# Optimization experiments

Hardware: AMD Instinct MI355X
Metric: run time of the kernel (lower is better)

## Reference

```python
import jax, jax.numpy as jnp
import numpy as np

NUM_FREQ = 32
MAX_POS = 10000.0
COORD_DIM = 3
EMB_DIM = COORD_DIM * NUM_FREQ * 2  # 192
KIN = 2 * EMB_DIM                   # 384
C = 32
T = 4
N_Y = 50000
N_X = 32768
K = 8
E = N_X * K
MLP_DIMS = [KIN, 128, 256, 128, C]


def sinusoidal_embed(p):
    # transformer-style sinusoidal embedding: [n, d] -> [n, d*NUM_FREQ*2]
    freqs = (1.0 / MAX_POS) ** (jnp.arange(NUM_FREQ, dtype=p.dtype) / NUM_FREQ)
    ang = p[..., None] * freqs                       # [n, d, nf]
    emb = jnp.stack([jnp.sin(ang), jnp.cos(ang)], axis=-1)  # [n, d, nf, 2]
    return emb.reshape(p.shape[0], -1)


def setup_inputs() -> dict:
    key = jax.random.key(0)
    ks = jax.random.split(key, 16)
    inp = {
        "y": jax.random.uniform(ks[0], (N_Y, COORD_DIM), dtype=jnp.float32),
        "x": jax.random.uniform(ks[1], (N_X, COORD_DIM), dtype=jnp.float32),
        "f_y": jax.random.normal(ks[2], (T, N_Y, C), dtype=jnp.float32),
        "neighbors_index": jax.random.randint(ks[3], (E,), 0, N_Y, dtype=jnp.int64),
    }
    # channel MLP params: 384 -> 128 -> 256 -> 128 -> 32, gelu between layers
    for i in range(4):
        fan_in, fan_out = MLP_DIMS[i], MLP_DIMS[i + 1]
        s = 1.0 / np.sqrt(fan_in)
        inp[f"W{i}"] = jax.random.uniform(ks[4 + 2 * i], (fan_in, fan_out), jnp.float32, -s, s)
        inp[f"b{i}"] = jax.random.uniform(ks[5 + 2 * i], (fan_out,), jnp.float32, -s, s)
    return inp


def reference(y, x, f_y, neighbors_index, W0, b0, W1, b1, W2, b2, W3, b3):
    n_x = x.shape[0]
    k = neighbors_index.shape[0] // n_x
    y_emb = sinusoidal_embed(y)            # [n_y, 192]
    x_emb = sinusoidal_embed(x)            # [n_x, 192]
    rep = y_emb[neighbors_index]           # [E, 192] gather per edge
    slf = jnp.repeat(x_emb, k, axis=0)     # [E, 192] query embedding per edge
    h = jnp.concatenate([rep, slf], axis=-1)  # [E, 384]
    h = jax.nn.gelu(h @ W0 + b0)
    h = jax.nn.gelu(h @ W1 + b1)
    h = jax.nn.gelu(h @ W2 + b2)
    kern = h @ W3 + b3                     # [E, C] kernel values
    in_feat = f_y[:, neighbors_index, :]   # [T, E, C] gathered source features
    prod = kern[None, :, :] * in_feat      # linear transform: k(x,y) * f(y)
    # reduction='sum' over each query's neighborhood (uniform K segments)
    out = prod.reshape(f_y.shape[0], n_x, k, -1).sum(axis=2)  # [T, n_x, C]
    return out
```

## Files before the change

### kernel.cpp

```cpp
#include <hip/hip_runtime.h>
#include <stdint.h>

#define EMB_DIM 192
#define KIN 384
#define CDIM 32
#define TDIM 4
#define N_Y 50000
#define N_X 32768
#define KNBR 8
#define ECNT (N_X*KNBR)

#define AS  200
#define H1S 134
#define H2S 262
#define KS  33

typedef __attribute__((ext_vector_type(8))) short bf16x8;
typedef __attribute__((ext_vector_type(4))) float f32x4;

static __device__ __forceinline__ short f2bf(float f){
  unsigned u = __float_as_uint(f);
  return (short)((u + 0x7FFFu) >> 16);
}
static __device__ __forceinline__ float geluf(float x){
  float x2 = x * x;
  float u  = __builtin_fmaf(0.044715f, x2, 1.0f);
  float p  = x * -1.5957691216057308f;
  float e  = __expf(p * u);
  return x * __builtin_amdgcn_rcpf(1.0f + e);
}

__global__ __launch_bounds__(256) void embed_all(const float* __restrict__ ypts,
                                                 const float* __restrict__ xpts,
                                                 short* __restrict__ emb){
  int id = blockIdx.x * 256 + threadIdx.x;
  int total = (N_Y + N_X) * 96;
  if (id >= total) return;
  int row = id / 96;
  int q = id - row * 96;
  int d = q >> 5, i = q & 31;
  float p = (row < N_Y) ? ypts[row * 3 + d] : xpts[(row - N_Y) * 3 + d];
  float f = __expf(-9.210340371976184f * (float)i * (1.0f / 32.0f));
  float s, c;
  __sincosf(p * f, &s, &c);
  unsigned u0 = __float_as_uint(s), u1 = __float_as_uint(c);
  unsigned pack = ((u0 + 0x7FFFu) >> 16) | (((u1 + 0x7FFFu) >> 16) << 16);
  *(unsigned*)&emb[(size_t)row * EMB_DIM + d * 64 + 2 * i] = pack;
}

__global__ __launch_bounds__(256) void transpose_all(
    const float* __restrict__ W0, const float* __restrict__ W1,
    const float* __restrict__ W2, const float* __restrict__ W3,
    short* __restrict__ w0t, short* __restrict__ w1t,
    short* __restrict__ w2t, short* __restrict__ w3t){
  int id = blockIdx.x * 256 + threadIdx.x;
  const float* src; short* dst; int K, N, loc;
  if      (id < 49152)  { src = W0; dst = w0t; K = 384; N = 128; loc = id; }
  else if (id < 81920)  { src = W1; dst = w1t; K = 128; N = 256; loc = id - 49152; }
  else if (id < 114688) { src = W2; dst = w2t; K = 256; N = 128; loc = id - 81920; }
  else if (id < 118784) { src = W3; dst = w3t; K = 128; N = 32;  loc = id - 114688; }
  else return;
  int n = loc / K, k = loc - n * K;
  dst[n * K + k] = f2bf(src[k * N + n]);
}

__global__ __launch_bounds__(256, 3) void fused_mlp(
    const short* __restrict__ yemb, const short* __restrict__ xemb,
    const int* __restrict__ nidx, const float* __restrict__ f_y,
    const short* __restrict__ w0t, const float* __restrict__ b0,
    const short* __restrict__ w1t, const float* __restrict__ b1,
    const short* __restrict__ w2t, const float* __restrict__ b2,
    const short* __restrict__ w3t, const float* __restrict__ b3,
    float* __restrict__ out)
{
  __shared__ __attribute__((aligned(16))) char smem[50688];
  short* s_a    = (short*)smem;
  short* s_h2   = (short*)smem;
  float* s_kern = (float*)smem;
  short* s_h1   = (short*)(smem + 33536);

  const int tid  = threadIdx.x;
  const int e0   = blockIdx.x * 64;
  const int wave = tid >> 6, lane = tid & 63;
  const int quad = lane >> 4, l15 = lane & 15;

  {
    const int r = tid >> 2, q = tid & 3;
    const int idx_r = nidx[e0 + r];
    const short* yrow = yemb + (size_t)idx_r * EMB_DIM + q * 48;
    uint4 v[6];
    #pragma unroll
    for (int i = 0; i < 6; ++i) v[i] = *(const uint4*)(yrow + i * 8);
    #pragma unroll
    for (int i = 0; i < 6; ++i)
      *(uint4*)&s_a[r * AS + q * 48 + i * 8] = v[i];
  }
  __syncthreads();

  {
    const short* xrow[4];
    #pragma unroll
    for (int mt = 0; mt < 4; ++mt)
      xrow[mt] = xemb + (size_t)((e0 + mt * 16 + l15) >> 3) * EMB_DIM + quad * 8;

    f32x4 acc0[4][2];
    #pragma unroll
    for (int mt = 0; mt < 4; ++mt)
      #pragma unroll
      for (int nt = 0; nt < 2; ++nt) acc0[mt][nt] = (f32x4){0.f, 0.f, 0.f, 0.f};

    #pragma unroll
    for (int ch = 0; ch < 12; ++ch) {
      bf16x8 a[4], b[2];
      #pragma unroll
      for (int mt = 0; mt < 4; ++mt) {
        if (ch < 6) a[mt] = *(const bf16x8*)&s_a[(mt * 16 + l15) * AS + ch * 32 + quad * 8];
        else        a[mt] = *(const bf16x8*)(xrow[mt] + (ch - 6) * 32);
      }
      #pragma unroll
      for (int nt = 0; nt < 2; ++nt)
        b[nt] = *(const bf16x8*)&w0t[(size_t)(wave * 32 + nt * 16 + l15) * 384 + ch * 32 + quad * 8];
      #pragma unroll
      for (int mt = 0; mt < 4; ++mt)
        #pragma unroll
        for (int nt = 0; nt < 2; ++nt)
          acc0[mt][nt] = __builtin_amdgcn_mfma_f32_16x16x32_bf16(a[mt], b[nt], acc0[mt][nt], 0, 0, 0);
    }
    #pragma unroll
    for (int nt = 0; nt < 2; ++nt) {
      int col = wave * 32 + nt * 16 + l15;
      float bias = b0[col];
      #pragma unroll
      for (int mt = 0; mt < 4; ++mt)
        #pragma unroll
        for (int rg = 0; rg < 4; ++rg) {
          int row = mt * 16 + quad * 4 + rg;
          s_h1[row * H1S + col] = f2bf(geluf(acc0[mt][nt][rg] + bias));
        }
    }
  }
  __syncthreads();

  {
    f32x4 acc1[4][4];
    #pragma unroll
    for (int mt = 0; mt < 4; ++mt)
      #pragma unroll
      for (int nt = 0; nt < 4; ++nt) acc1[mt][nt] = (f32x4){0.f, 0.f, 0.f, 0.f};
    #pragma unroll
    for (int ch = 0; ch < 4; ++ch) {
      bf16x8 a[4], b[4];
      #pragma unroll
      for (int mt = 0; mt < 4; ++mt)
        a[mt] = *(const bf16x8*)&s_h1[(mt * 16 + l15) * H1S + ch * 32 + quad * 8];
      #pragma unroll
      for (int nt = 0; nt < 4; ++nt)
        b[nt] = *(const bf16x8*)&w1t[(size_t)(wave * 64 + nt * 16 + l15) * 128 + ch * 32 + quad * 8];
      #pragma unroll
      for (int mt = 0; mt < 4; ++mt)
        #pragma unroll
        for (int nt = 0; nt < 4; ++nt)
          acc1[mt][nt] = __builtin_amdgcn_mfma_f32_16x16x32_bf16(a[mt], b[nt], acc1[mt][nt], 0, 0, 0);
    }
    #pragma unroll
    for (int nt = 0; nt < 4; ++nt) {
      int col = wave * 64 + nt * 16 + l15;
      float bias = b1[col];
      #pragma unroll
      for (int mt = 0; mt < 4; ++mt)
        #pragma unroll
        for (int rg = 0; rg < 4; ++rg) {
          int row = mt * 16 + quad * 4 + rg;
          s_h2[row * H2S + col] = f2bf(geluf(acc1[mt][nt][rg] + bias));
        }
    }
  }
  __syncthreads();

  {
    f32x4 acc2[4][2];
    #pragma unroll
    for (int mt = 0; mt < 4; ++mt)
      #pragma unroll
      for (int nt = 0; nt < 2; ++nt) acc2[mt][nt] = (f32x4){0.f, 0.f, 0.f, 0.f};
    #pragma unroll
    for (int ch = 0; ch < 8; ++ch) {
      bf16x8 a[4], b[2];
      #pragma unroll
      for (int mt = 0; mt < 4; ++mt)
        a[mt] = *(const bf16x8*)&s_h2[(mt * 16 + l15) * H2S + ch * 32 + quad * 8];
      #pragma unroll
      for (int nt = 0; nt < 2; ++nt)
        b[nt] = *(const bf16x8*)&w2t[(size_t)(wave * 32 + nt * 16 + l15) * 256 + ch * 32 + quad * 8];
      #pragma unroll
      for (int mt = 0; mt < 4; ++mt)
        #pragma unroll
        for (int nt = 0; nt < 2; ++nt)
          acc2[mt][nt] = __builtin_amdgcn_mfma_f32_16x16x32_bf16(a[mt], b[nt], acc2[mt][nt], 0, 0, 0);
    }
    #pragma unroll
    for (int nt = 0; nt < 2; ++nt) {
      int col = wave * 32 + nt * 16 + l15;
      float bias = b2[col];
      #pragma unroll
      for (int mt = 0; mt < 4; ++mt)
        #pragma unroll
        for (int rg = 0; rg < 4; ++rg) {
          int row = mt * 16 + quad * 4 + rg;
          s_h1[row * H1S + col] = f2bf(geluf(acc2[mt][nt][rg] + bias));
        }
    }
  }
  __syncthreads();

  {
    f32x4 acc3[2];
    acc3[0] = (f32x4){0.f, 0.f, 0.f, 0.f};
    acc3[1] = (f32x4){0.f, 0.f, 0.f, 0.f};
    #pragma unroll
    for (int ch = 0; ch < 4; ++ch) {
      bf16x8 a3 = *(const bf16x8*)&s_h1[(wave * 16 + l15) * H1S + ch * 32 + quad * 8];
      #pragma unroll
      for (int nt = 0; nt < 2; ++nt) {
        bf16x8 b3f = *(const bf16x8*)&w3t[(size_t)(nt * 16 + l15) * 128 + ch * 32 + quad * 8];
        acc3[nt] = __builtin_amdgcn_mfma_f32_16x16x32_bf16(a3, b3f, acc3[nt], 0, 0, 0);
      }
    }
    #pragma unroll
    for (int nt = 0; nt < 2; ++nt) {
      int col = nt * 16 + l15;
      float bias = b3[col];
      #pragma unroll
      for (int rg = 0; rg < 4; ++rg) {
        int row = wave * 16 + quad * 4 + rg;
        s_kern[row * KS + col] = acc3[nt][rg] + bias;
      }
    }
  }
  __syncthreads();

  {
    const int xloc = tid >> 5;
    const int c    = tid & 31;
    float acc[TDIM] = {0.f, 0.f, 0.f, 0.f};
    const int ebase = xloc * 8;
    #pragma unroll
    for (int j = 0; j < KNBR; ++j) {
      float kv = s_kern[(ebase + j) * KS + c];
      int idx = nidx[e0 + ebase + j];
      const float* fp = f_y + (size_t)idx * CDIM + c;
      #pragma unroll
      for (int t = 0; t < TDIM; ++t)
        acc[t] += kv * fp[(size_t)t * N_Y * CDIM];
    }
    const int xg = blockIdx.x * 8 + xloc;
    #pragma unroll
    for (int t = 0; t < TDIM; ++t)
      out[((size_t)t * N_X + xg) * CDIM + c] = acc[t];
  }
}

extern "C" void kernel_launch(void* const* d_in, const int* in_sizes, int n_in,
                              void* d_out, int out_size, void* d_ws, size_t ws_size,
                              hipStream_t stream)
{
  const float* y   = (const float*)d_in[0];
  const float* x   = (const float*)d_in[1];
  const float* f_y = (const float*)d_in[2];
  const int*  nidx = (const int*)d_in[3];
  const float* W0 = (const float*)d_in[4];  const float* b0 = (const float*)d_in[5];
  const float* W1 = (const float*)d_in[6];  const float* b1 = (const float*)d_in[7];
  const float* W2 = (const float*)d_in[8];  const float* b2 = (const float*)d_in[9];
  const float* W3 = (const float*)d_in[10]; const float* b3 = (const float*)d_in[11];

  char* ws = (char*)d_ws;
  short* yemb = (short*)(ws + 0);
  short* xemb = (short*)(ws + 19200000);
  short* w0t  = (short*)(ws + 31782912);
  short* w1t  = (short*)(ws + 31881216);
  short* w2t  = (short*)(ws + 31946752);
  short* w3t  = (short*)(ws + 32012288);

  hipLaunchKernelGGL(embed_all, dim3(((N_Y + N_X) * 96 + 255) / 256), dim3(256), 0, stream,
                     y, x, yemb);
  hipLaunchKernelGGL(transpose_all, dim3((118784 + 255) / 256), dim3(256), 0, stream,
                     W0, W1, W2, W3, w0t, w1t, w2t, w3t);
  hipLaunchKernelGGL(fused_mlp, dim3(ECNT / 64), dim3(256), 0, stream,
                     yemb, xemb, nidx, f_y, w0t, b0, w1t, b1, w2t, b2, w3t, b3,
                     (float*)d_out);
}
```

Before: 279.2 us.

## Split first MLP layer per point and precompute projected embeddings

The first linear layer is split into a y half and an x half. Each half is applied once per point (50k y points and 32k x points) in a new precompute kernel, instead of once per edge (262k edges). The edge kernel now only gathers the two 128-wide projected rows, adds them and applies GELU, which removes the K=384 first-layer GEMM from the per-edge work. In exchange, c_y is stored in bf16, which adds rounding before the addition, and c_x is stored in fp32, which makes the per-edge gather traffic larger.

```diff
diff --git a/kernel.cpp b/kernel.cpp
--- a/kernel.cpp
+++ b/kernel.cpp
@@ -2,7 +2,6 @@
 #include <stdint.h>
 
 #define EMB_DIM 192
-#define KIN 384
 #define CDIM 32
 #define TDIM 4
 #define N_Y 50000
@@ -10,10 +9,10 @@
 #define KNBR 8
 #define ECNT (N_X*KNBR)
 
-#define AS  200
 #define H1S 134
 #define H2S 262
 #define KS  33
+#define ES  200
 
 typedef __attribute__((ext_vector_type(8))) short bf16x8;
 typedef __attribute__((ext_vector_type(4))) float f32x4;
@@ -30,51 +29,109 @@
   return x * __builtin_amdgcn_rcpf(1.0f + e);
 }
 
-__global__ __launch_bounds__(256) void embed_all(const float* __restrict__ ypts,
-                                                 const float* __restrict__ xpts,
-                                                 short* __restrict__ emb){
-  int id = blockIdx.x * 256 + threadIdx.x;
-  int total = (N_Y + N_X) * 96;
-  if (id >= total) return;
-  int row = id / 96;
-  int q = id - row * 96;
-  int d = q >> 5, i = q & 31;
-  float p = (row < N_Y) ? ypts[row * 3 + d] : xpts[(row - N_Y) * 3 + d];
-  float f = __expf(-9.210340371976184f * (float)i * (1.0f / 32.0f));
-  float s, c;
-  __sincosf(p * f, &s, &c);
-  unsigned u0 = __float_as_uint(s), u1 = __float_as_uint(c);
-  unsigned pack = ((u0 + 0x7FFFu) >> 16) | (((u1 + 0x7FFFu) >> 16) << 16);
-  *(unsigned*)&emb[(size_t)row * EMB_DIM + d * 64 + 2 * i] = pack;
-}
-
 __global__ __launch_bounds__(256) void transpose_all(
     const float* __restrict__ W0, const float* __restrict__ W1,
     const float* __restrict__ W2, const float* __restrict__ W3,
-    short* __restrict__ w0t, short* __restrict__ w1t,
-    short* __restrict__ w2t, short* __restrict__ w3t){
+    short* __restrict__ w0yt, short* __restrict__ w0xt,
+    short* __restrict__ w1t, short* __restrict__ w2t, short* __restrict__ w3t){
   int id = blockIdx.x * 256 + threadIdx.x;
-  const float* src; short* dst; int K, N, loc;
-  if      (id < 49152)  { src = W0; dst = w0t; K = 384; N = 128; loc = id; }
-  else if (id < 81920)  { src = W1; dst = w1t; K = 128; N = 256; loc = id - 49152; }
-  else if (id < 114688) { src = W2; dst = w2t; K = 256; N = 128; loc = id - 81920; }
-  else if (id < 118784) { src = W3; dst = w3t; K = 128; N = 32;  loc = id - 114688; }
-  else return;
-  int n = loc / K, k = loc - n * K;
-  dst[n * K + k] = f2bf(src[k * N + n]);
-}
-
-__global__ __launch_bounds__(256, 3) void fused_mlp(
-    const short* __restrict__ yemb, const short* __restrict__ xemb,
+  if (id < 24576) {
+    int n = id / 192, k = id - n * 192;
+    w0yt[id] = f2bf(W0[k * 128 + n]);
+  } else if (id < 49152) {
+    int loc = id - 24576; int n = loc / 192, k = loc - n * 192;
+    w0xt[loc] = f2bf(W0[(k + 192) * 128 + n]);
+  } else if (id < 81920) {
+    int loc = id - 49152; int n = loc / 128, k = loc - n * 128;
+    w1t[loc] = f2bf(W1[k * 256 + n]);
+  } else if (id < 114688) {
+    int loc = id - 81920; int n = loc / 256, k = loc - n * 256;
+    w2t[loc] = f2bf(W2[k * 128 + n]);
+  } else if (id < 118784) {
+    int loc = id - 114688; int n = loc / 128, k = loc - n * 128;
+    w3t[loc] = f2bf(W3[k * 32 + n]);
+  }
+}
+
+__global__ __launch_bounds__(256, 2) void precompute_c(
+    const float* __restrict__ ypts, const float* __restrict__ xpts,
+    const short* __restrict__ w0yt, const short* __restrict__ w0xt,
+    const float* __restrict__ b0,
+    short* __restrict__ c_y, float* __restrict__ c_x)
+{
+  __shared__ __attribute__((aligned(16))) short s_e[64 * ES];
+  const int tid = threadIdx.x;
+  const bool isY = blockIdx.x < 782;
+  const int row0 = isY ? blockIdx.x * 64 : (blockIdx.x - 782) * 64;
+  const int wave = tid >> 6, lane = tid & 63;
+  const int quad = lane >> 4, l15 = lane & 15;
+
+  {
+    const int r = tid >> 2, q = tid & 3;
+    const int grow = row0 + r;
+    const bool valid = isY ? (grow < N_Y) : true;
+    const float* src = isY ? (ypts + (size_t)grow * 3) : (xpts + (size_t)grow * 3);
+    float c[3] = {0.f, 0.f, 0.f};
+    if (valid) { c[0] = src[0]; c[1] = src[1]; c[2] = src[2]; }
+    #pragma unroll
+    for (int j = 0; j < 24; ++j) {
+      int p = q * 24 + j;
+      int d = p >> 5, i = p & 31;
+      float f = __expf(-0.28782313662425575f * (float)i);
+      float s, co;
+      __sincosf(c[d] * f, &s, &co);
+      unsigned u0 = __float_as_uint(s), u1 = __float_as_uint(co);
+      unsigned pk = ((u0 + 0x7FFFu) >> 16) | (((u1 + 0x7FFFu) >> 16) << 16);
+      *(unsigned*)&s_e[r * ES + d * 64 + 2 * i] = pk;
+    }
+  }
+  __syncthreads();
+
+  const short* w0t = isY ? w0yt : w0xt;
+  f32x4 acc[4][2];
+  #pragma unroll
+  for (int mt = 0; mt < 4; ++mt)
+    #pragma unroll
+    for (int nt = 0; nt < 2; ++nt) acc[mt][nt] = (f32x4){0.f, 0.f, 0.f, 0.f};
+  #pragma unroll
+  for (int ch = 0; ch < 6; ++ch) {
+    bf16x8 a[4], b[2];
+    #pragma unroll
+    for (int mt = 0; mt < 4; ++mt)
+      a[mt] = *(const bf16x8*)&s_e[(mt * 16 + l15) * ES + ch * 32 + quad * 8];
+    #pragma unroll
+    for (int nt = 0; nt < 2; ++nt)
+      b[nt] = *(const bf16x8*)&w0t[(size_t)(wave * 32 + nt * 16 + l15) * 192 + ch * 32 + quad * 8];
+    #pragma unroll
+    for (int mt = 0; mt < 4; ++mt)
+      #pragma unroll
+      for (int nt = 0; nt < 2; ++nt)
+        acc[mt][nt] = __builtin_amdgcn_mfma_f32_16x16x32_bf16(a[mt], b[nt], acc[mt][nt], 0, 0, 0);
+  }
+  #pragma unroll
+  for (int nt = 0; nt < 2; ++nt) {
+    int col = wave * 32 + nt * 16 + l15;
+    float bias = isY ? 0.f : b0[col];
+    #pragma unroll
+    for (int mt = 0; mt < 4; ++mt)
+      #pragma unroll
+      for (int rg = 0; rg < 4; ++rg) {
+        int grow = row0 + mt * 16 + quad * 4 + rg;
+        if (isY) { if (grow < N_Y) c_y[(size_t)grow * 128 + col] = f2bf(acc[mt][nt][rg]); }
+        else     { c_x[(size_t)grow * 128 + col] = acc[mt][nt][rg] + bias; }
+      }
+  }
+}
+
+__global__ __launch_bounds__(256, 3) void fused_edge(
+    const short* __restrict__ c_y, const float* __restrict__ c_x,
     const int* __restrict__ nidx, const float* __restrict__ f_y,
-    const short* __restrict__ w0t, const float* __restrict__ b0,
     const short* __restrict__ w1t, const float* __restrict__ b1,
     const short* __restrict__ w2t, const float* __restrict__ b2,
     const short* __restrict__ w3t, const float* __restrict__ b3,
     float* __restrict__ out)
 {
   __shared__ __attribute__((aligned(16))) char smem[50688];
-  short* s_a    = (short*)smem;
   short* s_h2   = (short*)smem;
   float* s_kern = (float*)smem;
   short* s_h1   = (short*)(smem + 33536);
@@ -86,57 +143,26 @@
 
   {
     const int r = tid >> 2, q = tid & 3;
-    const int idx_r = nidx[e0 + r];
-    const short* yrow = yemb + (size_t)idx_r * EMB_DIM + q * 48;
-    uint4 v[6];
-    #pragma unroll
-    for (int i = 0; i < 6; ++i) v[i] = *(const uint4*)(yrow + i * 8);
-    #pragma unroll
-    for (int i = 0; i < 6; ++i)
-      *(uint4*)&s_a[r * AS + q * 48 + i * 8] = v[i];
-  }
-  __syncthreads();
-
-  {
-    const short* xrow[4];
-    #pragma unroll
-    for (int mt = 0; mt < 4; ++mt)
-      xrow[mt] = xemb + (size_t)((e0 + mt * 16 + l15) >> 3) * EMB_DIM + quad * 8;
-
-    f32x4 acc0[4][2];
-    #pragma unroll
-    for (int mt = 0; mt < 4; ++mt)
-      #pragma unroll
-      for (int nt = 0; nt < 2; ++nt) acc0[mt][nt] = (f32x4){0.f, 0.f, 0.f, 0.f};
-
-    #pragma unroll
-    for (int ch = 0; ch < 12; ++ch) {
-      bf16x8 a[4], b[2];
-      #pragma unroll
-      for (int mt = 0; mt < 4; ++mt) {
-        if (ch < 6) a[mt] = *(const bf16x8*)&s_a[(mt * 16 + l15) * AS + ch * 32 + quad * 8];
-        else        a[mt] = *(const bf16x8*)(xrow[mt] + (ch - 6) * 32);
-      }
-      #pragma unroll
-      for (int nt = 0; nt < 2; ++nt)
-        b[nt] = *(const bf16x8*)&w0t[(size_t)(wave * 32 + nt * 16 + l15) * 384 + ch * 32 + quad * 8];
-      #pragma unroll
-      for (int mt = 0; mt < 4; ++mt)
-        #pragma unroll
-        for (int nt = 0; nt < 2; ++nt)
-          acc0[mt][nt] = __builtin_amdgcn_mfma_f32_16x16x32_bf16(a[mt], b[nt], acc0[mt][nt], 0, 0, 0);
-    }
-    #pragma unroll
-    for (int nt = 0; nt < 2; ++nt) {
-      int col = wave * 32 + nt * 16 + l15;
-      float bias = b0[col];
-      #pragma unroll
-      for (int mt = 0; mt < 4; ++mt)
-        #pragma unroll
-        for (int rg = 0; rg < 4; ++rg) {
-          int row = mt * 16 + quad * 4 + rg;
-          s_h1[row * H1S + col] = f2bf(geluf(acc0[mt][nt][rg] + bias));
-        }
+    const int idx = nidx[e0 + r];
+    const uint4*  cyp = (const uint4*)(c_y + (size_t)idx * 128 + q * 32);
+    const float4* cxp = (const float4*)(c_x + (size_t)((e0 + r) >> 3) * 128 + q * 32);
+    uint4  cyv[4];
+    float4 cxv[8];
+    #pragma unroll
+    for (int i = 0; i < 4; ++i) cyv[i] = cyp[i];
+    #pragma unroll
+    for (int i = 0; i < 8; ++i) cxv[i] = cxp[i];
+    const float* cxa = (const float*)cxv;
+    const unsigned* cya = (const unsigned*)cyv;
+    unsigned* dst = (unsigned*)&s_h1[r * H1S + q * 32];
+    #pragma unroll
+    for (int jj = 0; jj < 16; ++jj) {
+      unsigned u = cya[jj];
+      float lo = __uint_as_float(u << 16)         + cxa[2 * jj];
+      float hi = __uint_as_float(u & 0xffff0000u) + cxa[2 * jj + 1];
+      unsigned pk = (unsigned)(unsigned short)f2bf(geluf(lo)) |
+                    ((unsigned)(unsigned short)f2bf(geluf(hi)) << 16);
+      dst[jj] = pk;
     }
   }
   __syncthreads();
@@ -274,18 +300,18 @@
   const float* W3 = (const float*)d_in[10]; const float* b3 = (const float*)d_in[11];
 
   char* ws = (char*)d_ws;
-  short* yemb = (short*)(ws + 0);
-  short* xemb = (short*)(ws + 19200000);
-  short* w0t  = (short*)(ws + 31782912);
-  short* w1t  = (short*)(ws + 31881216);
-  short* w2t  = (short*)(ws + 31946752);
-  short* w3t  = (short*)(ws + 32012288);
-
-  hipLaunchKernelGGL(embed_all, dim3(((N_Y + N_X) * 96 + 255) / 256), dim3(256), 0, stream,
-                     y, x, yemb);
+  short* c_y  = (short*)(ws + 0);
+  float* c_x  = (float*)(ws + 12800000);
+  short* w0yt = (short*)(ws + 29577216);
+  short* w0xt = (short*)(ws + 29626368);
+  short* w1t  = (short*)(ws + 29675520);
+  short* w2t  = (short*)(ws + 29741056);
+  short* w3t  = (short*)(ws + 29806592);
+
   hipLaunchKernelGGL(transpose_all, dim3((118784 + 255) / 256), dim3(256), 0, stream,
-                     W0, W1, W2, W3, w0t, w1t, w2t, w3t);
-  hipLaunchKernelGGL(fused_mlp, dim3(ECNT / 64), dim3(256), 0, stream,
-                     yemb, xemb, nidx, f_y, w0t, b0, w1t, b1, w2t, b2, w3t, b3,
-                     (float*)d_out);
-}
+                     W0, W1, W2, W3, w0yt, w0xt, w1t, w2t, w3t);
+  hipLaunchKernelGGL(precompute_c, dim3(782 + 512), dim3(256), 0, stream,
+                     y, x, w0yt, w0xt, b0, c_y, c_x);
+  hipLaunchKernelGGL(fused_edge, dim3(ECNT / 64), dim3(256), 0, stream,
+                     c_y, c_x, nidx, f_y, w1t, b1, w2t, b2, w3t, b3, (float*)d_out);
+}
```

After: 241.9 us. -13.3%, faster.
